# Optimization experiments

Measured on AMD Instinct MI355X. Metric: run time of the kernel, lower is better.

## Reference

```python
import jax, jax.numpy as jnp
import numpy as np

DIM = 512
HEADS = 8
DIM_HEAD = 64
INNER = HEADS * DIM_HEAD  # 512
NUM_PATCHES = 64
NUM_FRAMES = 32
EPS = 1e-5


def setup_inputs() -> dict:
    key = jax.random.key(0)
    k1, k2, k3, k4 = jax.random.split(key, 4)
    B, T = 4, NUM_PATCHES * NUM_FRAMES  # 4, 2048
    x = jax.random.normal(k1, (B, T, DIM), dtype=jnp.float32)
    w_qkv = jax.random.normal(k2, (DIM, 3 * INNER), dtype=jnp.float32) * (DIM ** -0.5)
    w_out = jax.random.normal(k3, (INNER, DIM), dtype=jnp.float32) * (INNER ** -0.5)
    b_out = jax.random.normal(k4, (DIM,), dtype=jnp.float32) * 0.01
    ln_g = jnp.ones((DIM,), dtype=jnp.float32)
    ln_b = jnp.zeros((DIM,), dtype=jnp.float32)
    return {"x": x, "ln_g": ln_g, "ln_b": ln_b, "w_qkv": w_qkv, "w_out": w_out, "b_out": b_out}


def _frame_causal_mask(T):
    # token i belongs to frame i // NUM_PATCHES; query frame attends to frames <= its own
    frame = jnp.arange(T) // NUM_PATCHES
    return frame[:, None] >= frame[None, :]  # [T, T] bool


def reference(x, ln_g, ln_b, w_qkv, w_out, b_out):
    B, T, C = x.shape
    scale = DIM_HEAD ** -0.5
    # LayerNorm
    mu = jnp.mean(x, axis=-1, keepdims=True)
    var = jnp.mean(jnp.square(x - mu), axis=-1, keepdims=True)
    xn = (x - mu) * jax.lax.rsqrt(var + EPS) * ln_g + ln_b
    # QKV projection (no bias)
    qkv = xn @ w_qkv  # [B, T, 3*INNER]
    q, k, v = jnp.split(qkv, 3, axis=-1)
    reshape = lambda t: t.reshape(B, T, HEADS, DIM_HEAD).transpose(0, 2, 1, 3)  # b h n d
    q, k, v = reshape(q), reshape(k), reshape(v)
    dots = jnp.einsum('bhqd,bhkd->bhqk', q, k) * scale
    mask = _frame_causal_mask(T)
    dots = jnp.where(mask[None, None], dots, -jnp.inf)
    attn = jax.nn.softmax(dots, axis=-1)
    out = jnp.einsum('bhqk,bhkd->bhqd', attn, v)
    out = out.transpose(0, 2, 1, 3).reshape(B, T, INNER)
    return out @ w_out + b_out
```

## Files before the change

kernel.cpp:

```cpp
#include <hip/hip_runtime.h>

typedef unsigned short u16;
typedef float f32x4 __attribute__((ext_vector_type(4)));
typedef short bf16x8 __attribute__((ext_vector_type(8)));

#define MFMA16(a, b, c) __builtin_amdgcn_mfma_f32_16x16x32_bf16((a), (b), (c), 0, 0, 0)
#define SWZ8(row, off) ((off) ^ (((row) & 7) << 3))

#define CFENCE() asm volatile("" ::: "memory")
#define BARRIER() do { CFENCE(); __builtin_amdgcn_s_barrier(); CFENCE(); } while (0)
#define VMW(n) asm volatile("s_waitcnt vmcnt(" #n ")" ::: "memory")

static __device__ __forceinline__ u16 f2bf(float f) {
  union { float f; unsigned u; } c; c.f = f;
  unsigned r = c.u + 0x7fffu + ((c.u >> 16) & 1u);
  return (u16)(r >> 16);
}

static __device__ __forceinline__ void llds16(u16* l, const u16* g) {
  __builtin_amdgcn_global_load_lds((const __attribute__((address_space(1))) void*)g,
                                   (__attribute__((address_space(3))) void*)l, 16, 0, 0);
}

__global__ __launch_bounds__(256) void prep_weights(
    const float* __restrict__ w_qkv, const float* __restrict__ w_out,
    u16* __restrict__ wqkvT, u16* __restrict__ woutT) {
  int idx = blockIdx.x * 256 + threadIdx.x;
  if (idx < 1536 * 512) {
    int n = idx >> 9, k = idx & 511;
    wqkvT[idx] = f2bf(w_qkv[k * 1536 + n]);
  } else {
    int j = idx - 1536 * 512;
    int n = j >> 9, k = j & 511;
    woutT[j] = f2bf(w_out[k * 512 + n]);
  }
}

__global__ __launch_bounds__(256) void ln_kernel(
    const float* __restrict__ x, const float* __restrict__ g,
    const float* __restrict__ be, u16* __restrict__ xn) {
  int row = blockIdx.x;
  int t = threadIdx.x;
  const float* xr = x + (size_t)row * 512;
  float2 v = *(const float2*)(xr + t * 2);
  float s = v.x + v.y, ss = v.x * v.x + v.y * v.y;
#pragma unroll
  for (int msk = 32; msk >= 1; msk >>= 1) {
    s += __shfl_xor(s, msk, 64);
    ss += __shfl_xor(ss, msk, 64);
  }
  __shared__ float red[8];
  int wv = t >> 6;
  if ((t & 63) == 0) { red[wv] = s; red[4 + wv] = ss; }
  __syncthreads();
  s = red[0] + red[1] + red[2] + red[3];
  ss = red[4] + red[5] + red[6] + red[7];
  float mu = s * (1.f / 512.f);
  float var = ss * (1.f / 512.f) - mu * mu;
  float rs = rsqrtf(var + 1e-5f);
  float a0 = (v.x - mu) * rs * g[2 * t] + be[2 * t];
  float a1 = (v.y - mu) * rs * g[2 * t + 1] + be[2 * t + 1];
  u16* o = xn + (size_t)row * 512 + t * 2;
  o[0] = f2bf(a0);
  o[1] = f2bf(a1);
}

__global__ __launch_bounds__(256) void gemm_qkv(
    const u16* __restrict__ A, const u16* __restrict__ BT,
    u16* __restrict__ qb, u16* __restrict__ kb, u16* __restrict__ vtb) {
  __shared__ u16 lsA[128 * 64], lsB[128 * 64];
  int m0 = blockIdx.x * 128, n0 = blockIdx.y * 128;
  int tid = threadIdx.x;
  int lane = tid & 63, wave = tid >> 6;
  int wm = (wave >> 1) * 64, wn = (wave & 1) * 64;
  int lr = lane & 15, lq = lane >> 4;
  f32x4 acc[4][4] = {};
  for (int kt = 0; kt < 8; ++kt) {
#pragma unroll
    for (int c = 0; c < 4; ++c) {
      int ci = c * 256 + tid;
      int row = ci >> 3, colb = ci & 7;
      int goff = kt * 64 + ((colb * 8) ^ ((row & 7) * 8));
      llds16(&lsA[ci * 8], &A[(size_t)(m0 + row) * 512 + goff]);
      llds16(&lsB[ci * 8], &BT[(size_t)(n0 + row) * 512 + goff]);
    }
    __syncthreads();
#pragma unroll
    for (int ks = 0; ks < 2; ++ks) {
      bf16x8 af[4], bfr[4];
#pragma unroll
      for (int i = 0; i < 4; ++i) {
        int ra = wm + i * 16 + lr;
        af[i] = *(const bf16x8*)&lsA[ra * 64 + SWZ8(ra, ks * 32 + lq * 8)];
        int rb = wn + i * 16 + lr;
        bfr[i] = *(const bf16x8*)&lsB[rb * 64 + SWZ8(rb, ks * 32 + lq * 8)];
      }
#pragma unroll
      for (int i = 0; i < 4; ++i)
#pragma unroll
        for (int j = 0; j < 4; ++j)
          acc[i][j] = MFMA16(af[i], bfr[j], acc[i][j]);
    }
    __syncthreads();
  }
#pragma unroll
  for (int j = 0; j < 4; ++j) {
    int gn = n0 + wn + j * 16 + lr;
    int sec = gn >> 9;
    int h = (gn >> 6) & 7;
    int d = gn & 63;
#pragma unroll
    for (int i = 0; i < 4; ++i) {
      int gm = m0 + wm + i * 16 + lq * 4;
      int b = gm >> 11, t0 = gm & 2047;
      int bh = b * 8 + h;
      if (sec == 0) {
#pragma unroll
        for (int r = 0; r < 4; ++r)
          qb[((size_t)bh * 2048 + t0 + r) * 64 + d] = f2bf(acc[i][j][r] * 0.125f);
      } else if (sec == 1) {
#pragma unroll
        for (int r = 0; r < 4; ++r)
          kb[((size_t)bh * 2048 + t0 + r) * 64 + d] = f2bf(acc[i][j][r]);
      } else {
        ushort4 pk;
        pk.x = f2bf(acc[i][j][0]);
        pk.y = f2bf(acc[i][j][1]);
        pk.z = f2bf(acc[i][j][2]);
        pk.w = f2bf(acc[i][j][3]);
        *(ushort4*)&vtb[((size_t)bh * 64 + d) * 2048 + t0] = pk;
      }
    }
  }
}

__global__ __launch_bounds__(256) void attn_kernel(
    const u16* __restrict__ qb, const u16* __restrict__ kb,
    const u16* __restrict__ vtb, u16* __restrict__ ao) {
  int blk = blockIdx.x;
  int xcd = blk & 7;
  int seq = blk >> 3;
  int bh = xcd * 4 + (seq & 3);
  int qf = 31 - (seq >> 2);
  int tid = threadIdx.x, lane = tid & 63, wave = tid >> 6;
  int lr = lane & 15, lq = lane >> 4;
  __shared__ u16 lsK[2][64 * 64], lsV[2][64 * 64];
  __shared__ u16 lsP[4][16 * 64];
  const u16* kfb = kb + (size_t)bh * 2048 * 64;
  const u16* vfb = vtb + (size_t)bh * 64 * 2048;

  int ci0 = tid, ci1 = 256 + tid;
  int r0 = ci0 >> 3, cb0 = ci0 & 7, sw0 = (cb0 * 8) ^ ((r0 & 7) * 8);
  int r1 = ci1 >> 3, cb1 = ci1 & 7, sw1 = (cb1 * 8) ^ ((r1 & 7) * 8);

#define STAGE(buf, kf_)                                                        \
  do {                                                                         \
    const u16* kp = kfb + (size_t)(kf_) * 64 * 64;                             \
    llds16(&lsK[buf][ci0 * 8], &kp[(size_t)r0 * 64 + sw0]);                    \
    llds16(&lsK[buf][ci1 * 8], &kp[(size_t)r1 * 64 + sw1]);                    \
    llds16(&lsV[buf][ci0 * 8], &vfb[(size_t)r0 * 2048 + (kf_) * 64 + sw0]);    \
    llds16(&lsV[buf][ci1 * 8], &vfb[(size_t)r1 * 2048 + (kf_) * 64 + sw1]);    \
  } while (0)

  STAGE(0, 0);

  const u16* qbase = qb + ((size_t)bh * 2048 + qf * 64) * 64;
  int qrow = wave * 16 + lr;
  bf16x8 qa0 = *(const bf16x8*)&qbase[qrow * 64 + lq * 8];
  bf16x8 qa1 = *(const bf16x8*)&qbase[qrow * 64 + 32 + lq * 8];

  f32x4 o[4] = {};
  float m = -1e30f, l = 0.f;

  for (int kf = 0; kf <= qf; ++kf) {
    int cur = kf & 1;
    if (kf < qf) {
      STAGE(cur ^ 1, kf + 1);
      VMW(4);
    } else {
      VMW(0);
    }
    BARRIER();
    f32x4 s[4];
    __builtin_amdgcn_s_setprio(1);
#pragma unroll
    for (int c = 0; c < 4; ++c) {
      int rk = c * 16 + lr;
      bf16x8 k0 = *(const bf16x8*)&lsK[cur][rk * 64 + SWZ8(rk, lq * 8)];
      bf16x8 k1 = *(const bf16x8*)&lsK[cur][rk * 64 + SWZ8(rk, 32 + lq * 8)];
      f32x4 z = {};
      z = MFMA16(k0, qa0, z);
      z = MFMA16(k1, qa1, z);
      s[c] = z;
    }
    __builtin_amdgcn_s_setprio(0);
    float m0 = fmaxf(fmaxf(s[0][0], s[0][1]), fmaxf(s[0][2], s[0][3]));
    float m1 = fmaxf(fmaxf(s[1][0], s[1][1]), fmaxf(s[1][2], s[1][3]));
    float m2 = fmaxf(fmaxf(s[2][0], s[2][1]), fmaxf(s[2][2], s[2][3]));
    float m3 = fmaxf(fmaxf(s[3][0], s[3][1]), fmaxf(s[3][2], s[3][3]));
    float mx = fmaxf(fmaxf(m0, m1), fmaxf(m2, m3));
    mx = fmaxf(mx, __shfl_xor(mx, 16, 64));
    mx = fmaxf(mx, __shfl_xor(mx, 32, 64));
    float mn = fmaxf(m, mx);
    float al = __expf(m - mn);
    m = mn;
    float sum = 0.f;
#pragma unroll
    for (int c = 0; c < 4; ++c) {
#pragma unroll
      for (int r = 0; r < 4; ++r) {
        s[c][r] = __expf(s[c][r] - mn);
        sum += s[c][r];
      }
    }
    sum += __shfl_xor(sum, 16, 64);
    sum += __shfl_xor(sum, 32, 64);
    l = l * al + sum;
    float al0 = __shfl(al, lq * 4 + 0, 64);
    float al1 = __shfl(al, lq * 4 + 1, 64);
    float al2 = __shfl(al, lq * 4 + 2, 64);
    float al3 = __shfl(al, lq * 4 + 3, 64);
#pragma unroll
    for (int oc = 0; oc < 4; ++oc) {
      o[oc][0] *= al0;
      o[oc][1] *= al1;
      o[oc][2] *= al2;
      o[oc][3] *= al3;
    }
    u16* pw = lsP[wave];
#pragma unroll
    for (int c = 0; c < 4; ++c) {
      union { u16 h[4]; uint2 q2; } pk;
      pk.h[0] = f2bf(s[c][0]);
      pk.h[1] = f2bf(s[c][1]);
      pk.h[2] = f2bf(s[c][2]);
      pk.h[3] = f2bf(s[c][3]);
      int kbase = c * 16 + lq * 4;
      *(uint2*)&pw[lr * 64 + (kbase ^ ((lr & 7) * 8))] = pk.q2;
    }
    bf16x8 pa0 = *(const bf16x8*)&pw[lr * 64 + SWZ8(lr, lq * 8)];
    bf16x8 pa1 = *(const bf16x8*)&pw[lr * 64 + SWZ8(lr, 32 + lq * 8)];
    __builtin_amdgcn_s_setprio(1);
#pragma unroll
    for (int oc = 0; oc < 4; ++oc) {
      int rv = oc * 16 + lr;
      bf16x8 v0 = *(const bf16x8*)&lsV[cur][rv * 64 + SWZ8(rv, lq * 8)];
      bf16x8 v1 = *(const bf16x8*)&lsV[cur][rv * 64 + SWZ8(rv, 32 + lq * 8)];
      o[oc] = MFMA16(pa0, v0, o[oc]);
      o[oc] = MFMA16(pa1, v1, o[oc]);
    }
    __builtin_amdgcn_s_setprio(0);
    BARRIER();
  }
#undef STAGE
  float inv = 1.0f / l;
  float i0 = __shfl(inv, lq * 4 + 0, 64);
  float i1 = __shfl(inv, lq * 4 + 1, 64);
  float i2 = __shfl(inv, lq * 4 + 2, 64);
  float i3 = __shfl(inv, lq * 4 + 3, 64);
  int b = bh >> 3, h = bh & 7;
#pragma unroll
  for (int oc = 0; oc < 4; ++oc) {
    int q = qf * 64 + wave * 16 + lq * 4;
    int col = h * 64 + oc * 16 + lr;
    ao[((size_t)b * 2048 + q + 0) * 512 + col] = f2bf(o[oc][0] * i0);
    ao[((size_t)b * 2048 + q + 1) * 512 + col] = f2bf(o[oc][1] * i1);
    ao[((size_t)b * 2048 + q + 2) * 512 + col] = f2bf(o[oc][2] * i2);
    ao[((size_t)b * 2048 + q + 3) * 512 + col] = f2bf(o[oc][3] * i3);
  }
}

__global__ __launch_bounds__(256) void gemm_out(
    const u16* __restrict__ A, const u16* __restrict__ BT,
    const float* __restrict__ bias, float* __restrict__ out) {
  __shared__ u16 lsA[128 * 64], lsB[128 * 64];
  int m0 = blockIdx.x * 128, n0 = blockIdx.y * 128;
  int tid = threadIdx.x;
  int lane = tid & 63, wave = tid >> 6;
  int wm = (wave >> 1) * 64, wn = (wave & 1) * 64;
  int lr = lane & 15, lq = lane >> 4;
  f32x4 acc[4][4] = {};
  for (int kt = 0; kt < 8; ++kt) {
#pragma unroll
    for (int c = 0; c < 4; ++c) {
      int ci = c * 256 + tid;
      int row = ci >> 3, colb = ci & 7;
      int goff = kt * 64 + ((colb * 8) ^ ((row & 7) * 8));
      llds16(&lsA[ci * 8], &A[(size_t)(m0 + row) * 512 + goff]);
      llds16(&lsB[ci * 8], &BT[(size_t)(n0 + row) * 512 + goff]);
    }
    __syncthreads();
#pragma unroll
    for (int ks = 0; ks < 2; ++ks) {
      bf16x8 af[4], bfr[4];
#pragma unroll
      for (int i = 0; i < 4; ++i) {
        int ra = wm + i * 16 + lr;
        af[i] = *(const bf16x8*)&lsA[ra * 64 + SWZ8(ra, ks * 32 + lq * 8)];
        int rb = wn + i * 16 + lr;
        bfr[i] = *(const bf16x8*)&lsB[rb * 64 + SWZ8(rb, ks * 32 + lq * 8)];
      }
#pragma unroll
      for (int i = 0; i < 4; ++i)
#pragma unroll
        for (int j = 0; j < 4; ++j)
          acc[i][j] = MFMA16(af[i], bfr[j], acc[i][j]);
    }
    __syncthreads();
  }
#pragma unroll
  for (int j = 0; j < 4; ++j) {
    int gn = n0 + wn + j * 16 + lr;
    float bj = bias[gn];
#pragma unroll
    for (int i = 0; i < 4; ++i) {
      int gm = m0 + wm + i * 16 + lq * 4;
#pragma unroll
      for (int r = 0; r < 4; ++r)
        out[(size_t)(gm + r) * 512 + gn] = acc[i][j][r] + bj;
    }
  }
}

extern "C" void kernel_launch(void* const* d_in, const int* in_sizes, int n_in,
                              void* d_out, int out_size, void* d_ws, size_t ws_size,
                              hipStream_t stream) {
  const float* x = (const float*)d_in[0];
  const float* ln_g = (const float*)d_in[1];
  const float* ln_b = (const float*)d_in[2];
  const float* w_qkv = (const float*)d_in[3];
  const float* w_out = (const float*)d_in[4];
  const float* b_out = (const float*)d_in[5];
  float* out = (float*)d_out;
  char* ws = (char*)d_ws;

  u16* xn    = (u16*)(ws + 0);
  u16* wqkvT = (u16*)(ws + 8388608);
  u16* woutT = (u16*)(ws + 9961472);
  u16* qb    = (u16*)(ws + 10485760);
  u16* kb    = (u16*)(ws + 18874368);
  u16* vtb   = (u16*)(ws + 27262976);
  u16* ao    = (u16*)(ws + 35651584);

  prep_weights<<<4096, 256, 0, stream>>>(w_qkv, w_out, wqkvT, woutT);
  ln_kernel<<<8192, 256, 0, stream>>>(x, ln_g, ln_b, xn);
  gemm_qkv<<<dim3(64, 12), 256, 0, stream>>>(xn, wqkvT, qb, kb, vtb);
  attn_kernel<<<1024, 256, 0, stream>>>(qb, kb, vtb, ao);
  gemm_out<<<dim3(64, 4), 256, 0, stream>>>(ao, woutT, b_out, out);
}
```

Baseline: 169.8 us.

## Pair causal query frames per attention block, use exp2 and packed bf16 converts

The attention kernel now handles two query frames per block (frame 31-p and frame p), so every block does the same amount of causal work and each staged K/V tile is reused for both frames. This halves the grid. Softmax switches to hardware exp2, with log2(e) folded into the Q scale, and probabilities are packed with v_cvt_pk_bf16_f32. The LayerNorm kernel is also rewritten to give one row per wave with vectorized float4 loads, removing the shared-memory reduction and the block barrier. The paired frames add register pressure and a divergent dual branch, and only 512 blocks remain to fill the GPU.

Result: no change. 171.1 us (+0.7%).

```diff
diff --git a/kernel.cpp b/kernel.cpp
--- a/kernel.cpp
+++ b/kernel.cpp
@@ -15,6 +15,18 @@
   union { float f; unsigned u; } c; c.f = f;
   unsigned r = c.u + 0x7fffu + ((c.u >> 16) & 1u);
   return (u16)(r >> 16);
+}
+
+static __device__ __forceinline__ float exp2_hw(float x) {
+  float r;
+  asm("v_exp_f32 %0, %1" : "=v"(r) : "v"(x));
+  return r;
+}
+
+static __device__ __forceinline__ unsigned cvtpk(float lo, float hi) {
+  unsigned r;
+  asm("v_cvt_pk_bf16_f32 %0, %1, %2" : "=v"(r) : "v"(lo), "v"(hi));
+  return r;
 }
 
 static __device__ __forceinline__ void llds16(u16* l, const u16* g) {
@@ -39,30 +51,34 @@
 __global__ __launch_bounds__(256) void ln_kernel(
     const float* __restrict__ x, const float* __restrict__ g,
     const float* __restrict__ be, u16* __restrict__ xn) {
-  int row = blockIdx.x;
-  int t = threadIdx.x;
-  const float* xr = x + (size_t)row * 512;
-  float2 v = *(const float2*)(xr + t * 2);
-  float s = v.x + v.y, ss = v.x * v.x + v.y * v.y;
+  int row = blockIdx.x * 4 + (threadIdx.x >> 6);
+  int lane = threadIdx.x & 63;
+  const float4* xr = (const float4*)(x + (size_t)row * 512) + lane * 2;
+  float4 v0 = xr[0], v1 = xr[1];
+  float s = v0.x + v0.y + v0.z + v0.w + v1.x + v1.y + v1.z + v1.w;
+  float ss = v0.x * v0.x + v0.y * v0.y + v0.z * v0.z + v0.w * v0.w +
+             v1.x * v1.x + v1.y * v1.y + v1.z * v1.z + v1.w * v1.w;
 #pragma unroll
   for (int msk = 32; msk >= 1; msk >>= 1) {
     s += __shfl_xor(s, msk, 64);
     ss += __shfl_xor(ss, msk, 64);
   }
-  __shared__ float red[8];
-  int wv = t >> 6;
-  if ((t & 63) == 0) { red[wv] = s; red[4 + wv] = ss; }
-  __syncthreads();
-  s = red[0] + red[1] + red[2] + red[3];
-  ss = red[4] + red[5] + red[6] + red[7];
   float mu = s * (1.f / 512.f);
   float var = ss * (1.f / 512.f) - mu * mu;
   float rs = rsqrtf(var + 1e-5f);
-  float a0 = (v.x - mu) * rs * g[2 * t] + be[2 * t];
-  float a1 = (v.y - mu) * rs * g[2 * t + 1] + be[2 * t + 1];
-  u16* o = xn + (size_t)row * 512 + t * 2;
-  o[0] = f2bf(a0);
-  o[1] = f2bf(a1);
+  const float4* gp = (const float4*)g + lane * 2;
+  const float4* bp = (const float4*)be + lane * 2;
+  float4 g0 = gp[0], g1 = gp[1], b0 = bp[0], b1 = bp[1];
+  union { u16 h[8]; uint4 q; } o;
+  o.h[0] = f2bf((v0.x - mu) * rs * g0.x + b0.x);
+  o.h[1] = f2bf((v0.y - mu) * rs * g0.y + b0.y);
+  o.h[2] = f2bf((v0.z - mu) * rs * g0.z + b0.z);
+  o.h[3] = f2bf((v0.w - mu) * rs * g0.w + b0.w);
+  o.h[4] = f2bf((v1.x - mu) * rs * g1.x + b1.x);
+  o.h[5] = f2bf((v1.y - mu) * rs * g1.y + b1.y);
+  o.h[6] = f2bf((v1.z - mu) * rs * g1.z + b1.z);
+  o.h[7] = f2bf((v1.w - mu) * rs * g1.w + b1.w);
+  *(uint4*)&xn[(size_t)row * 512 + lane * 8] = o.q;
 }
 
 __global__ __launch_bounds__(256) void gemm_qkv(
@@ -117,7 +133,7 @@
       if (sec == 0) {
 #pragma unroll
         for (int r = 0; r < 4; ++r)
-          qb[((size_t)bh * 2048 + t0 + r) * 64 + d] = f2bf(acc[i][j][r] * 0.125f);
+          qb[((size_t)bh * 2048 + t0 + r) * 64 + d] = f2bf(acc[i][j][r] * 0.180336880f);
       } else if (sec == 1) {
 #pragma unroll
         for (int r = 0; r < 4; ++r)
@@ -141,7 +157,8 @@
   int xcd = blk & 7;
   int seq = blk >> 3;
   int bh = xcd * 4 + (seq & 3);
-  int qf = 31 - (seq >> 2);
+  int pair = seq >> 2;
+  int qfA = 31 - pair, qfB = pair;
   int tid = threadIdx.x, lane = tid & 63, wave = tid >> 6;
   int lr = lane & 15, lq = lane >> 4;
   __shared__ u16 lsK[2][64 * 64], lsV[2][64 * 64];
@@ -164,109 +181,184 @@
 
   STAGE(0, 0);
 
-  const u16* qbase = qb + ((size_t)bh * 2048 + qf * 64) * 64;
   int qrow = wave * 16 + lr;
-  bf16x8 qa0 = *(const bf16x8*)&qbase[qrow * 64 + lq * 8];
-  bf16x8 qa1 = *(const bf16x8*)&qbase[qrow * 64 + 32 + lq * 8];
-
-  f32x4 o[4] = {};
-  float m = -1e30f, l = 0.f;
-
-  for (int kf = 0; kf <= qf; ++kf) {
+  const u16* qbA = qb + ((size_t)bh * 2048 + qfA * 64) * 64;
+  const u16* qbB = qb + ((size_t)bh * 2048 + qfB * 64) * 64;
+  bf16x8 qaA0 = *(const bf16x8*)&qbA[qrow * 64 + lq * 8];
+  bf16x8 qaA1 = *(const bf16x8*)&qbA[qrow * 64 + 32 + lq * 8];
+  bf16x8 qaB0 = *(const bf16x8*)&qbB[qrow * 64 + lq * 8];
+  bf16x8 qaB1 = *(const bf16x8*)&qbB[qrow * 64 + 32 + lq * 8];
+
+  f32x4 oA[4] = {}, oB[4] = {};
+  float mA = -1e30f, lA = 0.f, mB = -1e30f, lB = 0.f;
+  u16* pw = lsP[wave];
+
+  for (int kf = 0; kf <= qfA; ++kf) {
     int cur = kf & 1;
-    if (kf < qf) {
+    bool dual = (kf <= qfB);
+    if (kf < qfA) {
       STAGE(cur ^ 1, kf + 1);
       VMW(4);
     } else {
       VMW(0);
     }
     BARRIER();
-    f32x4 s[4];
+    f32x4 sA[4], sB[4];
     __builtin_amdgcn_s_setprio(1);
 #pragma unroll
     for (int c = 0; c < 4; ++c) {
       int rk = c * 16 + lr;
       bf16x8 k0 = *(const bf16x8*)&lsK[cur][rk * 64 + SWZ8(rk, lq * 8)];
       bf16x8 k1 = *(const bf16x8*)&lsK[cur][rk * 64 + SWZ8(rk, 32 + lq * 8)];
-      f32x4 z = {};
-      z = MFMA16(k0, qa0, z);
-      z = MFMA16(k1, qa1, z);
-      s[c] = z;
+      f32x4 zA = {};
+      zA = MFMA16(k0, qaA0, zA);
+      zA = MFMA16(k1, qaA1, zA);
+      sA[c] = zA;
+      if (dual) {
+        f32x4 zB = {};
+        zB = MFMA16(k0, qaB0, zB);
+        zB = MFMA16(k1, qaB1, zB);
+        sB[c] = zB;
+      }
     }
     __builtin_amdgcn_s_setprio(0);
-    float m0 = fmaxf(fmaxf(s[0][0], s[0][1]), fmaxf(s[0][2], s[0][3]));
-    float m1 = fmaxf(fmaxf(s[1][0], s[1][1]), fmaxf(s[1][2], s[1][3]));
-    float m2 = fmaxf(fmaxf(s[2][0], s[2][1]), fmaxf(s[2][2], s[2][3]));
-    float m3 = fmaxf(fmaxf(s[3][0], s[3][1]), fmaxf(s[3][2], s[3][3]));
-    float mx = fmaxf(fmaxf(m0, m1), fmaxf(m2, m3));
-    mx = fmaxf(mx, __shfl_xor(mx, 16, 64));
-    mx = fmaxf(mx, __shfl_xor(mx, 32, 64));
-    float mn = fmaxf(m, mx);
-    float al = __expf(m - mn);
-    m = mn;
-    float sum = 0.f;
-#pragma unroll
-    for (int c = 0; c < 4; ++c) {
-#pragma unroll
-      for (int r = 0; r < 4; ++r) {
-        s[c][r] = __expf(s[c][r] - mn);
-        sum += s[c][r];
-      }
-    }
-    sum += __shfl_xor(sum, 16, 64);
-    sum += __shfl_xor(sum, 32, 64);
-    l = l * al + sum;
-    float al0 = __shfl(al, lq * 4 + 0, 64);
-    float al1 = __shfl(al, lq * 4 + 1, 64);
-    float al2 = __shfl(al, lq * 4 + 2, 64);
-    float al3 = __shfl(al, lq * 4 + 3, 64);
-#pragma unroll
-    for (int oc = 0; oc < 4; ++oc) {
-      o[oc][0] *= al0;
-      o[oc][1] *= al1;
-      o[oc][2] *= al2;
-      o[oc][3] *= al3;
-    }
-    u16* pw = lsP[wave];
-#pragma unroll
-    for (int c = 0; c < 4; ++c) {
-      union { u16 h[4]; uint2 q2; } pk;
-      pk.h[0] = f2bf(s[c][0]);
-      pk.h[1] = f2bf(s[c][1]);
-      pk.h[2] = f2bf(s[c][2]);
-      pk.h[3] = f2bf(s[c][3]);
-      int kbase = c * 16 + lq * 4;
-      *(uint2*)&pw[lr * 64 + (kbase ^ ((lr & 7) * 8))] = pk.q2;
-    }
-    bf16x8 pa0 = *(const bf16x8*)&pw[lr * 64 + SWZ8(lr, lq * 8)];
-    bf16x8 pa1 = *(const bf16x8*)&pw[lr * 64 + SWZ8(lr, 32 + lq * 8)];
+
+    bf16x8 paA0, paA1, paB0, paB1;
+    {
+      float m0 = fmaxf(fmaxf(sA[0][0], sA[0][1]), fmaxf(sA[0][2], sA[0][3]));
+      float m1 = fmaxf(fmaxf(sA[1][0], sA[1][1]), fmaxf(sA[1][2], sA[1][3]));
+      float m2 = fmaxf(fmaxf(sA[2][0], sA[2][1]), fmaxf(sA[2][2], sA[2][3]));
+      float m3 = fmaxf(fmaxf(sA[3][0], sA[3][1]), fmaxf(sA[3][2], sA[3][3]));
+      float mx = fmaxf(fmaxf(m0, m1), fmaxf(m2, m3));
+      mx = fmaxf(mx, __shfl_xor(mx, 16, 64));
+      mx = fmaxf(mx, __shfl_xor(mx, 32, 64));
+      float mn = fmaxf(mA, mx);
+      float al = exp2_hw(mA - mn);
+      mA = mn;
+      float sum = 0.f;
+#pragma unroll
+      for (int c = 0; c < 4; ++c)
+#pragma unroll
+        for (int r = 0; r < 4; ++r) {
+          sA[c][r] = exp2_hw(sA[c][r] - mn);
+          sum += sA[c][r];
+        }
+      sum += __shfl_xor(sum, 16, 64);
+      sum += __shfl_xor(sum, 32, 64);
+      lA = lA * al + sum;
+      float al0 = __shfl(al, lq * 4 + 0, 64);
+      float al1 = __shfl(al, lq * 4 + 1, 64);
+      float al2 = __shfl(al, lq * 4 + 2, 64);
+      float al3 = __shfl(al, lq * 4 + 3, 64);
+#pragma unroll
+      for (int oc = 0; oc < 4; ++oc) {
+        oA[oc][0] *= al0;
+        oA[oc][1] *= al1;
+        oA[oc][2] *= al2;
+        oA[oc][3] *= al3;
+      }
+#pragma unroll
+      for (int c = 0; c < 4; ++c) {
+        union { unsigned u[2]; uint2 q2; } pk;
+        pk.u[0] = cvtpk(sA[c][0], sA[c][1]);
+        pk.u[1] = cvtpk(sA[c][2], sA[c][3]);
+        *(uint2*)&pw[lr * 64 + ((c * 16 + lq * 4) ^ ((lr & 7) * 8))] = pk.q2;
+      }
+      paA0 = *(const bf16x8*)&pw[lr * 64 + SWZ8(lr, lq * 8)];
+      paA1 = *(const bf16x8*)&pw[lr * 64 + SWZ8(lr, 32 + lq * 8)];
+    }
+    if (dual) {
+      float m0 = fmaxf(fmaxf(sB[0][0], sB[0][1]), fmaxf(sB[0][2], sB[0][3]));
+      float m1 = fmaxf(fmaxf(sB[1][0], sB[1][1]), fmaxf(sB[1][2], sB[1][3]));
+      float m2 = fmaxf(fmaxf(sB[2][0], sB[2][1]), fmaxf(sB[2][2], sB[2][3]));
+      float m3 = fmaxf(fmaxf(sB[3][0], sB[3][1]), fmaxf(sB[3][2], sB[3][3]));
+      float mx = fmaxf(fmaxf(m0, m1), fmaxf(m2, m3));
+      mx = fmaxf(mx, __shfl_xor(mx, 16, 64));
+      mx = fmaxf(mx, __shfl_xor(mx, 32, 64));
+      float mn = fmaxf(mB, mx);
+      float al = exp2_hw(mB - mn);
+      mB = mn;
+      float sum = 0.f;
+#pragma unroll
+      for (int c = 0; c < 4; ++c)
+#pragma unroll
+        for (int r = 0; r < 4; ++r) {
+          sB[c][r] = exp2_hw(sB[c][r] - mn);
+          sum += sB[c][r];
+        }
+      sum += __shfl_xor(sum, 16, 64);
+      sum += __shfl_xor(sum, 32, 64);
+      lB = lB * al + sum;
+      float al0 = __shfl(al, lq * 4 + 0, 64);
+      float al1 = __shfl(al, lq * 4 + 1, 64);
+      float al2 = __shfl(al, lq * 4 + 2, 64);
+      float al3 = __shfl(al, lq * 4 + 3, 64);
+#pragma unroll
+      for (int oc = 0; oc < 4; ++oc) {
+        oB[oc][0] *= al0;
+        oB[oc][1] *= al1;
+        oB[oc][2] *= al2;
+        oB[oc][3] *= al3;
+      }
+#pragma unroll
+      for (int c = 0; c < 4; ++c) {
+        union { unsigned u[2]; uint2 q2; } pk;
+        pk.u[0] = cvtpk(sB[c][0], sB[c][1]);
+        pk.u[1] = cvtpk(sB[c][2], sB[c][3]);
+        *(uint2*)&pw[lr * 64 + ((c * 16 + lq * 4) ^ ((lr & 7) * 8))] = pk.q2;
+      }
+      paB0 = *(const bf16x8*)&pw[lr * 64 + SWZ8(lr, lq * 8)];
+      paB1 = *(const bf16x8*)&pw[lr * 64 + SWZ8(lr, 32 + lq * 8)];
+    }
     __builtin_amdgcn_s_setprio(1);
 #pragma unroll
     for (int oc = 0; oc < 4; ++oc) {
       int rv = oc * 16 + lr;
       bf16x8 v0 = *(const bf16x8*)&lsV[cur][rv * 64 + SWZ8(rv, lq * 8)];
       bf16x8 v1 = *(const bf16x8*)&lsV[cur][rv * 64 + SWZ8(rv, 32 + lq * 8)];
-      o[oc] = MFMA16(pa0, v0, o[oc]);
-      o[oc] = MFMA16(pa1, v1, o[oc]);
+      oA[oc] = MFMA16(paA0, v0, oA[oc]);
+      oA[oc] = MFMA16(paA1, v1, oA[oc]);
+      if (dual) {
+        oB[oc] = MFMA16(paB0, v0, oB[oc]);
+        oB[oc] = MFMA16(paB1, v1, oB[oc]);
+      }
     }
     __builtin_amdgcn_s_setprio(0);
     BARRIER();
   }
 #undef STAGE
-  float inv = 1.0f / l;
-  float i0 = __shfl(inv, lq * 4 + 0, 64);
-  float i1 = __shfl(inv, lq * 4 + 1, 64);
-  float i2 = __shfl(inv, lq * 4 + 2, 64);
-  float i3 = __shfl(inv, lq * 4 + 3, 64);
   int b = bh >> 3, h = bh & 7;
-#pragma unroll
-  for (int oc = 0; oc < 4; ++oc) {
-    int q = qf * 64 + wave * 16 + lq * 4;
-    int col = h * 64 + oc * 16 + lr;
-    ao[((size_t)b * 2048 + q + 0) * 512 + col] = f2bf(o[oc][0] * i0);
-    ao[((size_t)b * 2048 + q + 1) * 512 + col] = f2bf(o[oc][1] * i1);
-    ao[((size_t)b * 2048 + q + 2) * 512 + col] = f2bf(o[oc][2] * i2);
-    ao[((size_t)b * 2048 + q + 3) * 512 + col] = f2bf(o[oc][3] * i3);
+  {
+    float inv = 1.0f / lA;
+    float i0 = __shfl(inv, lq * 4 + 0, 64);
+    float i1 = __shfl(inv, lq * 4 + 1, 64);
+    float i2 = __shfl(inv, lq * 4 + 2, 64);
+    float i3 = __shfl(inv, lq * 4 + 3, 64);
+#pragma unroll
+    for (int oc = 0; oc < 4; ++oc) {
+      int q = qfA * 64 + wave * 16 + lq * 4;
+      int col = h * 64 + oc * 16 + lr;
+      ao[((size_t)b * 2048 + q + 0) * 512 + col] = f2bf(oA[oc][0] * i0);
+      ao[((size_t)b * 2048 + q + 1) * 512 + col] = f2bf(oA[oc][1] * i1);
+      ao[((size_t)b * 2048 + q + 2) * 512 + col] = f2bf(oA[oc][2] * i2);
+      ao[((size_t)b * 2048 + q + 3) * 512 + col] = f2bf(oA[oc][3] * i3);
+    }
+  }
+  {
+    float inv = 1.0f / lB;
+    float i0 = __shfl(inv, lq * 4 + 0, 64);
+    float i1 = __shfl(inv, lq * 4 + 1, 64);
+    float i2 = __shfl(inv, lq * 4 + 2, 64);
+    float i3 = __shfl(inv, lq * 4 + 3, 64);
+#pragma unroll
+    for (int oc = 0; oc < 4; ++oc) {
+      int q = qfB * 64 + wave * 16 + lq * 4;
+      int col = h * 64 + oc * 16 + lr;
+      ao[((size_t)b * 2048 + q + 0) * 512 + col] = f2bf(oB[oc][0] * i0);
+      ao[((size_t)b * 2048 + q + 1) * 512 + col] = f2bf(oB[oc][1] * i1);
+      ao[((size_t)b * 2048 + q + 2) * 512 + col] = f2bf(oB[oc][2] * i2);
+      ao[((size_t)b * 2048 + q + 3) * 512 + col] = f2bf(oB[oc][3] * i3);
+    }
   }
 }
 
@@ -343,8 +435,8 @@
   u16* ao    = (u16*)(ws + 35651584);
 
   prep_weights<<<4096, 256, 0, stream>>>(w_qkv, w_out, wqkvT, woutT);
-  ln_kernel<<<8192, 256, 0, stream>>>(x, ln_g, ln_b, xn);
+  ln_kernel<<<2048, 256, 0, stream>>>(x, ln_g, ln_b, xn);
   gemm_qkv<<<dim3(64, 12), 256, 0, stream>>>(xn, wqkvT, qb, kb, vtb);
-  attn_kernel<<<1024, 256, 0, stream>>>(qb, kb, vtb, ao);
+  attn_kernel<<<512, 256, 0, stream>>>(qb, kb, vtb, ao);
   gemm_out<<<dim3(64, 4), 256, 0, stream>>>(ao, woutT, b_out, out);
 }
```

## Tile weight transpose, vectorize layernorm, XCD-aware GEMM order, exp2 softmax with packed bf16

Applied to the files above, without the earlier changes.

The weight prep becomes a shared-memory tiled transpose with coalesced float4 reads and 16-byte writes. LayerNorm now runs one row per wave, which removes the block reduction and barrier, and uses vector loads and stores. Both GEMMs remap a 1D grid so that blocks on the same XCD share A rows for better L2 reuse. In attention, log2(e) is folded into the Q scale so softmax can use the hardware exp2, and P is packed with v_cvt_pk_bf16_f32. This adds inline asm dependence and may change rounding slightly.

Measured after the change: 163.9 us. 3.5% less time.

```diff
diff --git a/kernel.cpp b/kernel.cpp
--- a/kernel.cpp
+++ b/kernel.cpp
@@ -17,6 +17,18 @@
   return (u16)(r >> 16);
 }
 
+static __device__ __forceinline__ float exp2_hw(float x) {
+  float r;
+  asm("v_exp_f32 %0, %1" : "=v"(r) : "v"(x));
+  return r;
+}
+
+static __device__ __forceinline__ unsigned cvtpk(float lo, float hi) {
+  unsigned r;
+  asm("v_cvt_pk_bf16_f32 %0, %1, %2" : "=v"(r) : "v"(lo), "v"(hi));
+  return r;
+}
+
 static __device__ __forceinline__ void llds16(u16* l, const u16* g) {
   __builtin_amdgcn_global_load_lds((const __attribute__((address_space(1))) void*)g,
                                    (__attribute__((address_space(3))) void*)l, 16, 0, 0);
@@ -25,51 +37,87 @@
 __global__ __launch_bounds__(256) void prep_weights(
     const float* __restrict__ w_qkv, const float* __restrict__ w_out,
     u16* __restrict__ wqkvT, u16* __restrict__ woutT) {
-  int idx = blockIdx.x * 256 + threadIdx.x;
-  if (idx < 1536 * 512) {
-    int n = idx >> 9, k = idx & 511;
-    wqkvT[idx] = f2bf(w_qkv[k * 1536 + n]);
+  __shared__ u16 tile[64][66];
+  int bid = blockIdx.x;
+  const float* src;
+  u16* dst;
+  int C, tr, tc;
+  if (bid < 192) {
+    src = w_qkv; dst = wqkvT; C = 1536;
+    tr = (bid & 7) * 64;
+    tc = (bid >> 3) * 64;
   } else {
-    int j = idx - 1536 * 512;
-    int n = j >> 9, k = j & 511;
-    woutT[j] = f2bf(w_out[k * 512 + n]);
+    int b2 = bid - 192;
+    src = w_out; dst = woutT; C = 512;
+    tr = (b2 & 7) * 64;
+    tc = (b2 >> 3) * 64;
+  }
+  int tid = threadIdx.x;
+  int i = tid >> 4;
+  int j4 = (tid & 15) * 4;
+#pragma unroll
+  for (int p = 0; p < 4; ++p) {
+    int row = i + p * 16;
+    float4 v = *(const float4*)&src[(size_t)(tr + row) * C + tc + j4];
+    tile[row][j4 + 0] = f2bf(v.x);
+    tile[row][j4 + 1] = f2bf(v.y);
+    tile[row][j4 + 2] = f2bf(v.z);
+    tile[row][j4 + 3] = f2bf(v.w);
+  }
+  __syncthreads();
+  int j = tid >> 3;
+  int i8 = (tid & 7) * 8;
+#pragma unroll
+  for (int p = 0; p < 2; ++p) {
+    int orow = j + p * 32;
+    union { u16 h[8]; uint4 q; } o;
+#pragma unroll
+    for (int s = 0; s < 8; ++s) o.h[s] = tile[i8 + s][orow];
+    *(uint4*)&dst[(size_t)(tc + orow) * 512 + tr + i8] = o.q;
   }
 }
 
 __global__ __launch_bounds__(256) void ln_kernel(
     const float* __restrict__ x, const float* __restrict__ g,
     const float* __restrict__ be, u16* __restrict__ xn) {
-  int row = blockIdx.x;
-  int t = threadIdx.x;
-  const float* xr = x + (size_t)row * 512;
-  float2 v = *(const float2*)(xr + t * 2);
-  float s = v.x + v.y, ss = v.x * v.x + v.y * v.y;
+  int row = blockIdx.x * 4 + (threadIdx.x >> 6);
+  int lane = threadIdx.x & 63;
+  const float4* xr = (const float4*)(x + (size_t)row * 512) + lane * 2;
+  float4 v0 = xr[0], v1 = xr[1];
+  float s = v0.x + v0.y + v0.z + v0.w + v1.x + v1.y + v1.z + v1.w;
+  float ss = v0.x * v0.x + v0.y * v0.y + v0.z * v0.z + v0.w * v0.w +
+             v1.x * v1.x + v1.y * v1.y + v1.z * v1.z + v1.w * v1.w;
 #pragma unroll
   for (int msk = 32; msk >= 1; msk >>= 1) {
     s += __shfl_xor(s, msk, 64);
     ss += __shfl_xor(ss, msk, 64);
   }
-  __shared__ float red[8];
-  int wv = t >> 6;
-  if ((t & 63) == 0) { red[wv] = s; red[4 + wv] = ss; }
-  __syncthreads();
-  s = red[0] + red[1] + red[2] + red[3];
-  ss = red[4] + red[5] + red[6] + red[7];
   float mu = s * (1.f / 512.f);
   float var = ss * (1.f / 512.f) - mu * mu;
   float rs = rsqrtf(var + 1e-5f);
-  float a0 = (v.x - mu) * rs * g[2 * t] + be[2 * t];
-  float a1 = (v.y - mu) * rs * g[2 * t + 1] + be[2 * t + 1];
-  u16* o = xn + (size_t)row * 512 + t * 2;
-  o[0] = f2bf(a0);
-  o[1] = f2bf(a1);
+  const float4* gp = (const float4*)g + lane * 2;
+  const float4* bp = (const float4*)be + lane * 2;
+  float4 g0 = gp[0], g1 = gp[1], b0 = bp[0], b1 = bp[1];
+  union { u16 h[8]; uint4 q; } o;
+  o.h[0] = f2bf((v0.x - mu) * rs * g0.x + b0.x);
+  o.h[1] = f2bf((v0.y - mu) * rs * g0.y + b0.y);
+  o.h[2] = f2bf((v0.z - mu) * rs * g0.z + b0.z);
+  o.h[3] = f2bf((v0.w - mu) * rs * g0.w + b0.w);
+  o.h[4] = f2bf((v1.x - mu) * rs * g1.x + b1.x);
+  o.h[5] = f2bf((v1.y - mu) * rs * g1.y + b1.y);
+  o.h[6] = f2bf((v1.z - mu) * rs * g1.z + b1.z);
+  o.h[7] = f2bf((v1.w - mu) * rs * g1.w + b1.w);
+  *(uint4*)&xn[(size_t)row * 512 + lane * 8] = o.q;
 }
 
 __global__ __launch_bounds__(256) void gemm_qkv(
     const u16* __restrict__ A, const u16* __restrict__ BT,
     u16* __restrict__ qb, u16* __restrict__ kb, u16* __restrict__ vtb) {
   __shared__ u16 lsA[128 * 64], lsB[128 * 64];
-  int m0 = blockIdx.x * 128, n0 = blockIdx.y * 128;
+  int bid = blockIdx.x;
+  int xcd = bid & 7, sq = bid >> 3;
+  int m0 = (xcd * 8 + (sq & 7)) * 128;
+  int n0 = (sq >> 3) * 128;
   int tid = threadIdx.x;
   int lane = tid & 63, wave = tid >> 6;
   int wm = (wave >> 1) * 64, wn = (wave & 1) * 64;
@@ -117,7 +165,7 @@
       if (sec == 0) {
 #pragma unroll
         for (int r = 0; r < 4; ++r)
-          qb[((size_t)bh * 2048 + t0 + r) * 64 + d] = f2bf(acc[i][j][r] * 0.125f);
+          qb[((size_t)bh * 2048 + t0 + r) * 64 + d] = f2bf(acc[i][j][r] * 0.180336880f);
       } else if (sec == 1) {
 #pragma unroll
         for (int r = 0; r < 4; ++r)
@@ -171,6 +219,7 @@
 
   f32x4 o[4] = {};
   float m = -1e30f, l = 0.f;
+  u16* pw = lsP[wave];
 
   for (int kf = 0; kf <= qf; ++kf) {
     int cur = kf & 1;
@@ -202,14 +251,14 @@
     mx = fmaxf(mx, __shfl_xor(mx, 16, 64));
     mx = fmaxf(mx, __shfl_xor(mx, 32, 64));
     float mn = fmaxf(m, mx);
-    float al = __expf(m - mn);
+    float al = exp2_hw(m - mn);
     m = mn;
     float sum = 0.f;
 #pragma unroll
     for (int c = 0; c < 4; ++c) {
 #pragma unroll
       for (int r = 0; r < 4; ++r) {
-        s[c][r] = __expf(s[c][r] - mn);
+        s[c][r] = exp2_hw(s[c][r] - mn);
         sum += s[c][r];
       }
     }
@@ -227,16 +276,12 @@
       o[oc][2] *= al2;
       o[oc][3] *= al3;
     }
-    u16* pw = lsP[wave];
-#pragma unroll
-    for (int c = 0; c < 4; ++c) {
-      union { u16 h[4]; uint2 q2; } pk;
-      pk.h[0] = f2bf(s[c][0]);
-      pk.h[1] = f2bf(s[c][1]);
-      pk.h[2] = f2bf(s[c][2]);
-      pk.h[3] = f2bf(s[c][3]);
-      int kbase = c * 16 + lq * 4;
-      *(uint2*)&pw[lr * 64 + (kbase ^ ((lr & 7) * 8))] = pk.q2;
+#pragma unroll
+    for (int c = 0; c < 4; ++c) {
+      union { unsigned u[2]; uint2 q2; } pk;
+      pk.u[0] = cvtpk(s[c][0], s[c][1]);
+      pk.u[1] = cvtpk(s[c][2], s[c][3]);
+      *(uint2*)&pw[lr * 64 + ((c * 16 + lq * 4) ^ ((lr & 7) * 8))] = pk.q2;
     }
     bf16x8 pa0 = *(const bf16x8*)&pw[lr * 64 + SWZ8(lr, lq * 8)];
     bf16x8 pa1 = *(const bf16x8*)&pw[lr * 64 + SWZ8(lr, 32 + lq * 8)];
@@ -274,7 +319,10 @@
     const u16* __restrict__ A, const u16* __restrict__ BT,
     const float* __restrict__ bias, float* __restrict__ out) {
   __shared__ u16 lsA[128 * 64], lsB[128 * 64];
-  int m0 = blockIdx.x * 128, n0 = blockIdx.y * 128;
+  int bid = blockIdx.x;
+  int xcd = bid & 7, sq = bid >> 3;
+  int m0 = (xcd * 8 + (sq & 7)) * 128;
+  int n0 = (sq >> 3) * 128;
   int tid = threadIdx.x;
   int lane = tid & 63, wave = tid >> 6;
   int wm = (wave >> 1) * 64, wn = (wave & 1) * 64;
@@ -342,9 +390,9 @@
   u16* vtb   = (u16*)(ws + 27262976);
   u16* ao    = (u16*)(ws + 35651584);
 
-  prep_weights<<<4096, 256, 0, stream>>>(w_qkv, w_out, wqkvT, woutT);
-  ln_kernel<<<8192, 256, 0, stream>>>(x, ln_g, ln_b, xn);
-  gemm_qkv<<<dim3(64, 12), 256, 0, stream>>>(xn, wqkvT, qb, kb, vtb);
+  prep_weights<<<256, 256, 0, stream>>>(w_qkv, w_out, wqkvT, woutT);
+  ln_kernel<<<2048, 256, 0, stream>>>(x, ln_g, ln_b, xn);
+  gemm_qkv<<<768, 256, 0, stream>>>(xn, wqkvT, qb, kb, vtb);
   attn_kernel<<<1024, 256, 0, stream>>>(qb, kb, vtb, ao);
-  gemm_out<<<dim3(64, 4), 256, 0, stream>>>(ao, woutT, b_out, out);
-}
+  gemm_out<<<256, 256, 0, stream>>>(ao, woutT, b_out, out);
+}
```
